# Kernel tuning notes

Measured on AMD Instinct MI355X. Metric: run time of the kernel, lower is better.

Reference implementation:

```python
import jax, jax.numpy as jnp
import numpy as np

V = 50000
E = 800000
HIDDEN = 128
NUM_BASES = 64
D_MIN, D_MAX = 0.0, 25.0  # squared-distance range for radius=5.0


def setup_inputs() -> dict:
    key = jax.random.key(0)
    ks = jax.random.split(key, 10)
    s = 1.0 / np.sqrt(HIDDEN)
    sb = 1.0 / np.sqrt(NUM_BASES)
    return {
        "X": jax.random.normal(ks[0], (V, HIDDEN), jnp.float32),
        "R": jax.random.normal(ks[1], (V, 3), jnp.float32),
        "src": jax.random.randint(ks[2], (E,), 0, V),
        "dest": jax.random.randint(ks[3], (E,), 0, V),
        # filter-generating MLP (no bias, per nn.Linear(..., bias=False))
        "W1": jax.random.uniform(ks[4], (NUM_BASES, HIDDEN), jnp.float32, -sb, sb),
        "W2": jax.random.uniform(ks[5], (HIDDEN, HIDDEN), jnp.float32, -s, s),
        # update MLP (with bias)
        "U1": jax.random.uniform(ks[6], (HIDDEN, HIDDEN), jnp.float32, -s, s),
        "b1": jax.random.uniform(ks[7], (HIDDEN,), jnp.float32, -s, s),
        "U2": jax.random.uniform(ks[8], (HIDDEN, HIDDEN), jnp.float32, -s, s),
        "b2": jax.random.uniform(ks[9], (HIDDEN,), jnp.float32, -s, s),
    }


def _rbf(d):
    # Gaussian RBF expansion: centers linspaced over [D_MIN, D_MAX]
    centers = jnp.linspace(D_MIN, D_MAX, NUM_BASES, dtype=d.dtype)
    width = (D_MAX - D_MIN) / (NUM_BASES - 1)
    return jnp.exp(-((d[:, None] - centers) ** 2) / (2.0 * width * width))  # [E, num_bases]


def reference(X, R, src, dest, W1, W2, U1, b1, U2, b2):
    # squared pairwise distance per edge (original: .square().sum(-1), no sqrt)
    D_ij = jnp.sum((R[src] - R[dest]) ** 2, axis=-1)  # [E]
    # filter-generating network: RBF -> Linear -> ReLU -> Linear -> ReLU
    M = jax.nn.relu(_rbf(D_ij) @ W1)
    M = jax.nn.relu(M @ W2)  # [E, d_h]
    # gather-multiply-scatter: continuous-filter convolution
    H = jax.ops.segment_sum(X[src] * M, dest, num_segments=X.shape[0])  # [V, d_h]
    # update MLP (note: self.W(X) in the original is dead code, overwritten)
    out = jax.nn.relu(H @ U1 + b1) @ U2 + b2
    return out
```

## Files before the change

### kernel.cpp

```cpp
#include <hip/hip_runtime.h>
#include <hip/hip_bf16.h>
#include <hip/hip_fp16.h>

#define HIDDEN 128
#define NB 64
#define TG 8192
#define TPTS (TG + 1)
#define TMAX 32.0f
#define TINV ((float)TG / TMAX)
#define CAP 64
#define NB1 1024
#define BINCAP 20

typedef _Float16 f16;
typedef _Float16 f16x8 __attribute__((ext_vector_type(8)));
typedef float floatx4 __attribute__((ext_vector_type(4)));
typedef unsigned short ushort;
typedef unsigned int uint;

__global__ __launch_bounds__(256) void megaprep(
    const int* __restrict__ src, const int* __restrict__ dest,
    const float* __restrict__ R, float4* __restrict__ Rp,
    const float* __restrict__ X, f16* __restrict__ Xh,
    const float* __restrict__ W1, const float* __restrict__ W2,
    f16* __restrict__ Th,
    const float* __restrict__ U1, const float* __restrict__ U2,
    f16* __restrict__ U1p, f16* __restrict__ U2p,
    uint* __restrict__ staging, uint* __restrict__ cnt1,
    int E, int V, int XB, int TB, int RB, int EPB) {
    __shared__ uint smem[256 + 256 * BINCAP];
    const int b = blockIdx.x;
    const int tid = threadIdx.x;
    if (b < NB1) {
        uint* scur = smem;
        uint* sbin = smem + 256;
        scur[tid] = 0;
        __syncthreads();
        const int e0 = b * EPB;
        const int e1 = min(e0 + EPB, E);
        for (int e = e0 + tid; e < e1; e += 256) {
            const uint s = (uint)src[e];
            const uint d = (uint)dest[e];
            const uint bin = d >> 8;
            const uint k = atomicAdd(&scur[bin], 1u);
            if (k < BINCAP) sbin[bin * BINCAP + k] = s | ((d & 255u) << 16);
        }
        __syncthreads();
        const uint n = min(scur[tid], (uint)BINCAP);
        uint4* dst = (uint4*)(staging + ((size_t)b * 256 + tid) * BINCAP);
        const uint4* sp = (const uint4*)(sbin + tid * BINCAP);
        for (uint k4 = 0; k4 * 4 < n; ++k4) dst[k4] = sp[k4];
        cnt1[b * 256 + tid] = n;
    } else if (b < NB1 + XB) {
        const int idx = ((b - NB1) * 256 + tid) * 8;
        if (idx < V * HIDDEN) {
            const float4 v0 = *(const float4*)(X + idx);
            const float4 v1 = *(const float4*)(X + idx + 4);
            f16x8 h;
            h[0] = (f16)v0.x; h[1] = (f16)v0.y; h[2] = (f16)v0.z; h[3] = (f16)v0.w;
            h[4] = (f16)v1.x; h[5] = (f16)v1.y; h[6] = (f16)v1.z; h[7] = (f16)v1.w;
            *(f16x8*)(Xh + idx) = h;
        }
    } else if (b < NB1 + XB + TB) {
        f16* h2 = (f16*)smem;
        const int lane = tid & 63;
        const int w = tid >> 6;
        const int rt = w & 1;
        const int ct0 = (w >> 1) * 4;
        const int lrow = lane & 15;
        const int lk = lane >> 4;
        const int g0 = (b - NB1 - XB) * 32;
        const float d2a = (float)(g0 + rt * 16 + lrow) * (TMAX / (float)TG);
        const float wid = 25.0f / 63.0f;
        f16x8 a[4];
#pragma unroll
        for (int kt = 0; kt < 2; ++kt)
#pragma unroll
            for (int j = 0; j < 8; ++j) {
                const float z = d2a - wid * (float)(kt * 32 + lk * 8 + j);
                a[kt][j] = (f16)expf(-(z * z) / (2.0f * wid * wid));
            }
        floatx4 acc[4];
#pragma unroll
        for (int c = 0; c < 4; ++c) acc[c] = (floatx4){0.f, 0.f, 0.f, 0.f};
#pragma unroll
        for (int c = 0; c < 4; ++c) {
            const int col = (ct0 + c) * 16 + lrow;
#pragma unroll
            for (int kt = 0; kt < 2; ++kt) {
                f16x8 bf;
#pragma unroll
                for (int j = 0; j < 8; ++j)
                    bf[j] = (f16)W1[(kt * 32 + lk * 8 + j) * HIDDEN + col];
                acc[c] = __builtin_amdgcn_mfma_f32_16x16x32_f16(a[kt], bf, acc[c], 0, 0, 0);
            }
        }
#pragma unroll
        for (int c = 0; c < 4; ++c) {
            const int col = (ct0 + c) * 16 + lrow;
#pragma unroll
            for (int rr = 0; rr < 4; ++rr)
                h2[(rt * 16 + lk * 4 + rr) * 136 + col] = (f16)fmaxf(acc[c][rr], 0.0f);
        }
        __syncthreads();
        f16x8 a2[4];
#pragma unroll
        for (int kt = 0; kt < 4; ++kt)
            a2[kt] = *(const f16x8*)&h2[(rt * 16 + lrow) * 136 + kt * 32 + lk * 8];
#pragma unroll
        for (int c = 0; c < 4; ++c) acc[c] = (floatx4){0.f, 0.f, 0.f, 0.f};
#pragma unroll
        for (int c = 0; c < 4; ++c) {
            const int col = (ct0 + c) * 16 + lrow;
#pragma unroll
            for (int kt = 0; kt < 4; ++kt) {
                f16x8 bf;
#pragma unroll
                for (int j = 0; j < 8; ++j)
                    bf[j] = (f16)W2[(kt * 32 + lk * 8 + j) * HIDDEN + col];
                acc[c] = __builtin_amdgcn_mfma_f32_16x16x32_f16(a2[kt], bf, acc[c], 0, 0, 0);
            }
        }
#pragma unroll
        for (int c = 0; c < 4; ++c) {
            const int col = (ct0 + c) * 16 + lrow;
#pragma unroll
            for (int rr = 0; rr < 4; ++rr) {
                const int g = g0 + rt * 16 + lk * 4 + rr;
                if (g <= TG) Th[(size_t)g * 128 + col] = (f16)fmaxf(acc[c][rr], 0.0f);
            }
        }
    } else if (b < NB1 + XB + TB + RB) {
        const int v = (b - NB1 - XB - TB) * 256 + tid;
        if (v < V) Rp[v] = make_float4(R[3 * v], R[3 * v + 1], R[3 * v + 2], 0.f);
    } else {
        const int ub = b - NB1 - XB - TB - RB;
        const int i = (ub & 63) * 256 + tid;
        const int j = i & 7;
        const int l = (i >> 3) & 63;
        const int ktct = i >> 9;
        const int kt = ktct >> 3, ct = ktct & 7;
        const int srcidx = (kt * 32 + (l >> 4) * 8 + j) * HIDDEN + ct * 16 + (l & 15);
        if (ub < 64) U1p[i] = (f16)U1[srcidx];
        else         U2p[i] = (f16)U2[srcidx];
    }
}

__global__ __launch_bounds__(256) void bucketize(
    const uint* __restrict__ staging, const uint* __restrict__ cnt1,
    ushort* __restrict__ eps, int* __restrict__ deg, int V) {
    __shared__ ushort bucket[256 * CAP];
    __shared__ uint lcur[256];
    const int r = blockIdx.x;
    const int tid = threadIdx.x;
    lcur[tid] = 0;
    __syncthreads();
    for (int b = tid; b < NB1; b += 256) {
        uint n = cnt1[b * 256 + r];
        n = min(n, (uint)BINCAP);
        const uint* seg = staging + ((size_t)b * 256 + r) * BINCAP;
        for (uint k = 0; k < n; ++k) {
            const uint e = seg[k];
            const uint dl = e >> 16;
            const uint kk = atomicAdd(&lcur[dl], 1u);
            if (kk < CAP) bucket[dl * CAP + kk] = (ushort)(e & 0xFFFFu);
        }
    }
    __syncthreads();
    const uint4* bs = (const uint4*)bucket;
    uint4* ed = (uint4*)(eps + (size_t)r * (256 * CAP));
    for (int i = tid; i < 256 * CAP / 8; i += 256) ed[i] = bs[i];
    const int d = r * 256 + tid;
    if (d < V) deg[d] = (int)min(lcur[tid], (uint)CAP);
}

__global__ __launch_bounds__(512) void gather_mlp(
    const int* __restrict__ deg, const ushort* __restrict__ eps,
    const float4* __restrict__ Rp,
    const f16* __restrict__ Xh, const f16* __restrict__ Th,
    const f16x8* __restrict__ U1p, const float* __restrict__ b1,
    const f16x8* __restrict__ U2p, const float* __restrict__ b2,
    float* __restrict__ out, int V) {
    __shared__ f16 hg[32 * 136];
    __shared__ f16 h2[32 * 136];
    const int tid = threadIdx.x;
    const int lane = tid & 63;
    const int wid = tid >> 6;
    const int nb = blockIdx.x * 32;

    const int cl = lane & 15;
    const int es = lane >> 4;
    const char* thb = (const char*)Th + cl * 16;
    const char* xhb = (const char*)Xh + cl * 16;
#pragma unroll
    for (int q = 0; q < 4; ++q) {
        const int lrowi = wid * 4 + q;
        const int node = nb + lrowi;
        const int dn = (node < V) ? deg[node] : 0;
        const float4 rn = Rp[min(node, V - 1)];
        float acc[8];
#pragma unroll
        for (int i = 0; i < 8; ++i) acc[i] = 0.0f;
        int my_s = 0;
        if (lane < dn) my_s = (int)eps[((size_t)node << 6) + lane];
        const float4 rs = Rp[my_s];
        const float dx = rs.x - rn.x;
        const float dy = rs.y - rn.y;
        const float dz = rs.z - rn.z;
        const float D2 = fmaf(dx, dx, fmaf(dy, dy, dz * dz));
        const int my_g = (lane < dn) ? min((int)fmaf(D2, TINV, 0.5f), TG) : TG;
        const int nst2 = (((dn + 3) >> 2) + 1) & ~1;
        for (int j = 0; j < nst2; j += 2) {
            const int idx0 = 4 * j + es;
            const int idx1 = idx0 + 4;
            const int s0 = __shfl(my_s, idx0);
            const int g0 = __shfl(my_g, idx0);
            const int s1 = __shfl(my_s, idx1);
            const int g1 = __shfl(my_g, idx1);
            const f16x8 m0 = *(const f16x8*)(thb + g0 * 256);
            const f16x8 x0 = *(const f16x8*)(xhb + s0 * 256);
            const f16x8 m1 = *(const f16x8*)(thb + g1 * 256);
            const f16x8 x1 = *(const f16x8*)(xhb + s1 * 256);
#pragma unroll
            for (int i = 0; i < 8; ++i)
                acc[i] = fmaf((float)m0[i], (float)x0[i], acc[i]);
#pragma unroll
            for (int i = 0; i < 8; ++i)
                acc[i] = fmaf((float)m1[i], (float)x1[i], acc[i]);
        }
#pragma unroll
        for (int i = 0; i < 8; ++i) {
            acc[i] += __shfl_xor(acc[i], 16);
            acc[i] += __shfl_xor(acc[i], 32);
        }
        if (es == 0) {
            f16x8 h;
#pragma unroll
            for (int i = 0; i < 8; ++i) h[i] = (f16)acc[i];
            *(f16x8*)&hg[lrowi * 136 + cl * 8] = h;
        }
    }
    __syncthreads();

    const int rt = wid & 1;
    const int ctp = wid >> 1;
    const int lrow = lane & 15;
    const int lk = lane >> 4;

    f16x8 a[4];
#pragma unroll
    for (int kt = 0; kt < 4; ++kt)
        a[kt] = *(const f16x8*)&hg[(rt * 16 + lrow) * 136 + kt * 32 + lk * 8];
    floatx4 acc2[2];
#pragma unroll
    for (int c = 0; c < 2; ++c) acc2[c] = (floatx4){0.f, 0.f, 0.f, 0.f};
#pragma unroll
    for (int c = 0; c < 2; ++c) {
        const int ct = ctp * 2 + c;
#pragma unroll
        for (int kt = 0; kt < 4; ++kt) {
            const f16x8 bf = U1p[(kt * 8 + ct) * 64 + lane];
            acc2[c] = __builtin_amdgcn_mfma_f32_16x16x32_f16(a[kt], bf, acc2[c], 0, 0, 0);
        }
    }
#pragma unroll
    for (int c = 0; c < 2; ++c) {
        const int col = (ctp * 2 + c) * 16 + lrow;
        const float bb = b1[col];
#pragma unroll
        for (int rr = 0; rr < 4; ++rr) {
            const int row = rt * 16 + lk * 4 + rr;
            h2[row * 136 + col] = (f16)fmaxf(acc2[c][rr] + bb, 0.0f);
        }
    }
    __syncthreads();

#pragma unroll
    for (int kt = 0; kt < 4; ++kt)
        a[kt] = *(const f16x8*)&h2[(rt * 16 + lrow) * 136 + kt * 32 + lk * 8];
#pragma unroll
    for (int c = 0; c < 2; ++c) acc2[c] = (floatx4){0.f, 0.f, 0.f, 0.f};
#pragma unroll
    for (int c = 0; c < 2; ++c) {
        const int ct = ctp * 2 + c;
#pragma unroll
        for (int kt = 0; kt < 4; ++kt) {
            const f16x8 bf = U2p[(kt * 8 + ct) * 64 + lane];
            acc2[c] = __builtin_amdgcn_mfma_f32_16x16x32_f16(a[kt], bf, acc2[c], 0, 0, 0);
        }
    }
#pragma unroll
    for (int c = 0; c < 2; ++c) {
        const int col = (ctp * 2 + c) * 16 + lrow;
        const float bb = b2[col];
#pragma unroll
        for (int rr = 0; rr < 4; ++rr) {
            const int row = nb + rt * 16 + lk * 4 + rr;
            if (row < V) out[(size_t)row * HIDDEN + col] = acc2[c][rr] + bb;
        }
    }
}

extern "C" void kernel_launch(void* const* d_in, const int* in_sizes, int n_in,
                              void* d_out, int out_size, void* d_ws, size_t ws_size,
                              hipStream_t stream) {
    const float* X = (const float*)d_in[0];
    const float* R = (const float*)d_in[1];
    const int* src = (const int*)d_in[2];
    const int* dest = (const int*)d_in[3];
    const float* W1 = (const float*)d_in[4];
    const float* W2 = (const float*)d_in[5];
    const float* U1 = (const float*)d_in[6];
    const float* b1 = (const float*)d_in[7];
    const float* U2 = (const float*)d_in[8];
    const float* b2 = (const float*)d_in[9];

    const int V = in_sizes[0] / HIDDEN;
    const int E = in_sizes[2];
    const int XB = (V * HIDDEN / 8 + 255) / 256;
    const int TB = (TPTS + 31) / 32;
    const int RB = (V + 255) / 256;
    const int NR = (V + 255) >> 8;
    const int EPB = (E + NB1 - 1) / NB1;

    char* base = (char*)d_ws;
    f16* Th = (f16*)base;                       base += ((size_t)TPTS * 128 * sizeof(f16) + 255) & ~255;
    f16* Xh = (f16*)base;                       base += (size_t)V * HIDDEN * sizeof(f16);
    ushort* eps = (ushort*)base;                base += (size_t)NR * 256 * CAP * sizeof(ushort);
    float4* Rp = (float4*)base;                 base += (size_t)V * sizeof(float4);
    f16* U1p = (f16*)base;                      base += (size_t)HIDDEN * HIDDEN * sizeof(f16);
    f16* U2p = (f16*)base;                      base += (size_t)HIDDEN * HIDDEN * sizeof(f16);
    uint* staging = (uint*)base;                base += (size_t)NB1 * 256 * BINCAP * sizeof(uint);
    uint* cnt1 = (uint*)base;                   base += (size_t)NB1 * 256 * sizeof(uint);
    int* deg = (int*)base;                      base += (size_t)NR * 256 * sizeof(int);

    megaprep<<<NB1 + XB + TB + RB + 128, 256, 0, stream>>>(
        src, dest, R, Rp, X, Xh, W1, W2, Th, U1, U2, U1p, U2p,
        staging, cnt1, E, V, XB, TB, RB, EPB);
    bucketize<<<NR, 256, 0, stream>>>(staging, cnt1, eps, deg, V);
    gather_mlp<<<(V + 31) / 32, 512, 0, stream>>>(deg, eps, (const float4*)Rp,
                                                  Xh, Th, (const f16x8*)U1p, b1,
                                                  (const f16x8*)U2p, b2,
                                                  (float*)d_out, V);
}
```

Before: 95.99 us.

## Assign one node per wavefront in gather_mlp with 1024-thread blocks

The gather phase now has each of 16 wavefronts handle a single node, instead of 8 wavefronts each looping over 4 nodes. Blocks grow to 1024 threads and cover 16 nodes, so there are twice as many blocks. The goal is more independent gather latency in flight, with the serial per-wave node loop replaced by wave-level parallelism. The cost is that only half the waves do the two MFMA stages, the MLP weights are reloaded per 16 rows rather than per 32, and 1024-thread blocks may limit occupancy and stall on barriers.

Result: no change. 94.63 us (-1.4%).

```diff
diff --git a/kernel.cpp b/kernel.cpp
--- a/kernel.cpp
+++ b/kernel.cpp
@@ -174,28 +174,26 @@
     if (d < V) deg[d] = (int)min(lcur[tid], (uint)CAP);
 }
 
-__global__ __launch_bounds__(512) void gather_mlp(
+__global__ __launch_bounds__(1024) void gather_mlp(
     const int* __restrict__ deg, const ushort* __restrict__ eps,
     const float4* __restrict__ Rp,
     const f16* __restrict__ Xh, const f16* __restrict__ Th,
     const f16x8* __restrict__ U1p, const float* __restrict__ b1,
     const f16x8* __restrict__ U2p, const float* __restrict__ b2,
     float* __restrict__ out, int V) {
-    __shared__ f16 hg[32 * 136];
-    __shared__ f16 h2[32 * 136];
+    __shared__ f16 hg[16 * 136];
+    __shared__ f16 h2[16 * 136];
     const int tid = threadIdx.x;
     const int lane = tid & 63;
     const int wid = tid >> 6;
-    const int nb = blockIdx.x * 32;
-
-    const int cl = lane & 15;
-    const int es = lane >> 4;
-    const char* thb = (const char*)Th + cl * 16;
-    const char* xhb = (const char*)Xh + cl * 16;
-#pragma unroll
-    for (int q = 0; q < 4; ++q) {
-        const int lrowi = wid * 4 + q;
-        const int node = nb + lrowi;
+    const int nb = blockIdx.x * 16;
+
+    {
+        const int cl = lane & 15;
+        const int es = lane >> 4;
+        const char* thb = (const char*)Th + cl * 16;
+        const char* xhb = (const char*)Xh + cl * 16;
+        const int node = nb + wid;
         const int dn = (node < V) ? deg[node] : 0;
         const float4 rn = Rp[min(node, V - 1)];
         float acc[8];
@@ -237,66 +235,50 @@
             f16x8 h;
 #pragma unroll
             for (int i = 0; i < 8; ++i) h[i] = (f16)acc[i];
-            *(f16x8*)&hg[lrowi * 136 + cl * 8] = h;
+            *(f16x8*)&hg[wid * 136 + cl * 8] = h;
         }
     }
     __syncthreads();
 
-    const int rt = wid & 1;
-    const int ctp = wid >> 1;
     const int lrow = lane & 15;
     const int lk = lane >> 4;
-
-    f16x8 a[4];
-#pragma unroll
-    for (int kt = 0; kt < 4; ++kt)
-        a[kt] = *(const f16x8*)&hg[(rt * 16 + lrow) * 136 + kt * 32 + lk * 8];
-    floatx4 acc2[2];
-#pragma unroll
-    for (int c = 0; c < 2; ++c) acc2[c] = (floatx4){0.f, 0.f, 0.f, 0.f};
-#pragma unroll
-    for (int c = 0; c < 2; ++c) {
-        const int ct = ctp * 2 + c;
+    if (wid < 8) {
+        const int ct = wid;
+        f16x8 a[4];
+#pragma unroll
+        for (int kt = 0; kt < 4; ++kt)
+            a[kt] = *(const f16x8*)&hg[lrow * 136 + kt * 32 + lk * 8];
+        floatx4 acc = (floatx4){0.f, 0.f, 0.f, 0.f};
 #pragma unroll
         for (int kt = 0; kt < 4; ++kt) {
             const f16x8 bf = U1p[(kt * 8 + ct) * 64 + lane];
-            acc2[c] = __builtin_amdgcn_mfma_f32_16x16x32_f16(a[kt], bf, acc2[c], 0, 0, 0);
-        }
-    }
-#pragma unroll
-    for (int c = 0; c < 2; ++c) {
-        const int col = (ctp * 2 + c) * 16 + lrow;
+            acc = __builtin_amdgcn_mfma_f32_16x16x32_f16(a[kt], bf, acc, 0, 0, 0);
+        }
+        const int col = ct * 16 + lrow;
         const float bb = b1[col];
 #pragma unroll
-        for (int rr = 0; rr < 4; ++rr) {
-            const int row = rt * 16 + lk * 4 + rr;
-            h2[row * 136 + col] = (f16)fmaxf(acc2[c][rr] + bb, 0.0f);
-        }
+        for (int rr = 0; rr < 4; ++rr)
+            h2[(lk * 4 + rr) * 136 + col] = (f16)fmaxf(acc[rr] + bb, 0.0f);
     }
     __syncthreads();
-
-#pragma unroll
-    for (int kt = 0; kt < 4; ++kt)
-        a[kt] = *(const f16x8*)&h2[(rt * 16 + lrow) * 136 + kt * 32 + lk * 8];
-#pragma unroll
-    for (int c = 0; c < 2; ++c) acc2[c] = (floatx4){0.f, 0.f, 0.f, 0.f};
-#pragma unroll
-    for (int c = 0; c < 2; ++c) {
-        const int ct = ctp * 2 + c;
+    if (wid < 8) {
+        const int ct = wid;
+        f16x8 a[4];
+#pragma unroll
+        for (int kt = 0; kt < 4; ++kt)
+            a[kt] = *(const f16x8*)&h2[lrow * 136 + kt * 32 + lk * 8];
+        floatx4 acc = (floatx4){0.f, 0.f, 0.f, 0.f};
 #pragma unroll
         for (int kt = 0; kt < 4; ++kt) {
             const f16x8 bf = U2p[(kt * 8 + ct) * 64 + lane];
-            acc2[c] = __builtin_amdgcn_mfma_f32_16x16x32_f16(a[kt], bf, acc2[c], 0, 0, 0);
-        }
-    }
-#pragma unroll
-    for (int c = 0; c < 2; ++c) {
-        const int col = (ctp * 2 + c) * 16 + lrow;
+            acc = __builtin_amdgcn_mfma_f32_16x16x32_f16(a[kt], bf, acc, 0, 0, 0);
+        }
+        const int col = ct * 16 + lrow;
         const float bb = b2[col];
 #pragma unroll
         for (int rr = 0; rr < 4; ++rr) {
-            const int row = nb + rt * 16 + lk * 4 + rr;
-            if (row < V) out[(size_t)row * HIDDEN + col] = acc2[c][rr] + bb;
+            const int row = nb + lk * 4 + rr;
+            if (row < V) out[(size_t)row * HIDDEN + col] = acc[rr] + bb;
         }
     }
 }
@@ -338,8 +320,8 @@
         src, dest, R, Rp, X, Xh, W1, W2, Th, U1, U2, U1p, U2p,
         staging, cnt1, E, V, XB, TB, RB, EPB);
     bucketize<<<NR, 256, 0, stream>>>(staging, cnt1, eps, deg, V);
-    gather_mlp<<<(V + 31) / 32, 512, 0, stream>>>(deg, eps, (const float4*)Rp,
-                                                  Xh, Th, (const f16x8*)U1p, b1,
-                                                  (const f16x8*)U2p, b2,
-                                                  (float*)d_out, V);
+    gather_mlp<<<(V + 15) / 16, 1024, 0, stream>>>(deg, eps, (const float4*)Rp,
+                                                   Xh, Th, (const f16x8*)U1p, b1,
+                                                   (const f16x8*)U2p, b2,
+                                                   (float*)d_out, V);
 }
```
